# Optimization experiments

Measured on AMD Instinct MI355X. Metric: run time of the kernel, lower is better.

## Reference

```python
import jax, jax.numpy as jnp
import numpy as np

N, E, T, H, D_IN, D_OUT = 50000, 320000, 4, 4, 128, 128
NEG_SLOPE = 0.2
LN_EPS = 1e-5


def setup_inputs() -> dict:
    key = jax.random.key(0)
    ks = jax.random.split(key, 10)
    x = jax.random.normal(ks[0], (N, D_IN), jnp.float32)
    edge_index = jax.random.randint(ks[1], (2, E), 0, N, jnp.int32)
    edge_attr = jax.random.randint(ks[2], (E,), 0, T, jnp.int32)
    W_gat = jax.random.normal(ks[3], (T, D_IN, H * D_OUT), jnp.float32) / np.sqrt(D_IN)
    a_src = jax.random.normal(ks[4], (T, H, D_OUT), jnp.float32) / np.sqrt(D_OUT)
    a_dst = jax.random.normal(ks[5], (T, H, D_OUT), jnp.float32) / np.sqrt(D_OUT)
    b_gat = jnp.zeros((T, D_OUT), jnp.float32)
    edge_type_weights = jnp.ones((T,), jnp.float32) / T
    W_fuse = jax.random.normal(ks[6], (T * D_OUT, D_OUT), jnp.float32) / np.sqrt(T * D_OUT)
    b_fuse = jnp.zeros((D_OUT,), jnp.float32)
    ln_gamma = jnp.ones((D_OUT,), jnp.float32)
    ln_beta = jnp.zeros((D_OUT,), jnp.float32)
    return {"x": x, "edge_index": edge_index, "edge_attr": edge_attr,
            "W_gat": W_gat, "a_src": a_src, "a_dst": a_dst, "b_gat": b_gat,
            "edge_type_weights": edge_type_weights, "W_fuse": W_fuse,
            "b_fuse": b_fuse, "ln_gamma": ln_gamma, "ln_beta": ln_beta}


def _gat_one_type(x, src_all, dst_all, mask_all, W, a_s, a_d, b):
    # x: [N, D_in]; src_all/dst_all: [E+N] (type-mask + self-loops on all nodes)
    n = x.shape[0]
    h = (x @ W).reshape(n, H, D_OUT)                      # [N, H, D]
    alpha_s = jnp.sum(h * a_s, axis=-1)                   # [N, H]
    alpha_d = jnp.sum(h * a_d, axis=-1)                   # [N, H]
    logit = jax.nn.leaky_relu(alpha_s[src_all] + alpha_d[dst_all], NEG_SLOPE)  # [Ea, H]
    neg_inf = jnp.float32(-1e30)
    logit = jnp.where(mask_all[:, None], logit, neg_inf)
    m = jax.ops.segment_max(logit, dst_all, num_segments=n)   # [N, H] (self-loops ensure finite)
    ex = jnp.exp(logit - m[dst_all])
    ex = jnp.where(mask_all[:, None], ex, 0.0)
    denom = jax.ops.segment_sum(ex, dst_all, num_segments=n)  # [N, H]
    alpha = ex / denom[dst_all]                                # [Ea, H]
    msg = alpha[:, :, None] * h[src_all]                       # [Ea, H, D]
    out = jax.ops.segment_sum(msg, dst_all, num_segments=n)   # [N, H, D]
    return out.mean(axis=1) + b                                # concat=False -> head mean


def reference(x, edge_index, edge_attr, W_gat, a_src, a_dst, b_gat,
              edge_type_weights, W_fuse, b_fuse, ln_gamma, ln_beta):
    n = x.shape[0]
    self_idx = jnp.arange(n, dtype=edge_index.dtype)
    src_all = jnp.concatenate([edge_index[0], self_idx])
    dst_all = jnp.concatenate([edge_index[1], self_idx])
    outs = []
    for t in range(T):
        mask_all = jnp.concatenate([edge_attr == t, jnp.ones((n,), bool)])
        outs.append(_gat_one_type(x, src_all, dst_all, mask_all,
                                  W_gat[t], a_src[t], a_dst[t], b_gat[t]))
    w = jax.nn.softmax(edge_type_weights)
    x_cat = jnp.concatenate([outs[t] * w[t] for t in range(T)], axis=1)  # [N, T*D]
    y = x_cat @ W_fuse + b_fuse
    mu = jnp.mean(y, axis=-1, keepdims=True)
    var = jnp.var(y, axis=-1, keepdims=True)
    y = (y - mu) / jnp.sqrt(var + LN_EPS) * ln_gamma + ln_beta
    return jax.nn.relu(y)
```

## Files before the change

kernel.cpp:

```cpp
#include <hip/hip_runtime.h>
#include <hip/hip_bf16.h>

#define TT 4
#define HH 4
#define DD 128
#define KAGG 2048

typedef __attribute__((ext_vector_type(8))) short short8;
typedef __attribute__((ext_vector_type(4))) float f32x4;
typedef __attribute__((ext_vector_type(4))) unsigned int uint4v;

__device__ __forceinline__ float lrelu(float z) { return z > 0.f ? z : 0.2f * z; }
__device__ __forceinline__ float bf2f(unsigned short u) {
  union { unsigned int i; float f; } v; v.i = ((unsigned int)u) << 16; return v.f;
}
__device__ __forceinline__ unsigned short f2b(float f) {
  union { float f; unsigned int i; } u; u.f = f;
  unsigned int r = u.i + 0x7fff + ((u.i >> 16) & 1);
  return (unsigned short)(r >> 16);
}
__device__ __forceinline__ void unpack8v(uint4v u, float* hv) {
  hv[0] = bf2f((unsigned short)(u.x & 0xffff));
  hv[1] = bf2f((unsigned short)(u.x >> 16));
  hv[2] = bf2f((unsigned short)(u.y & 0xffff));
  hv[3] = bf2f((unsigned short)(u.y >> 16));
  hv[4] = bf2f((unsigned short)(u.z & 0xffff));
  hv[5] = bf2f((unsigned short)(u.z >> 16));
  hv[6] = bf2f((unsigned short)(u.w & 0xffff));
  hv[7] = bf2f((unsigned short)(u.w >> 16));
}

__global__ __launch_bounds__(256) void prologue_kernel(
    const float* __restrict__ x, unsigned short* __restrict__ xb, int total4,
    const float* __restrict__ Wg, const float* __restrict__ a_s,
    const float* __restrict__ a_d, const float* __restrict__ W_fuse,
    const float* __restrict__ b_gat, const float* __restrict__ etw,
    const float* __restrict__ b_fuse, unsigned short* __restrict__ Gfrag,
    unsigned short* __restrict__ Pall, float* __restrict__ cbias,
    const int* __restrict__ dst, const int* __restrict__ attr,
    int* __restrict__ deg, int E, int N) {
  int bid = blockIdx.x;
  const int nconv = (total4 + 255) >> 8;
  if (bid < nconv) {
    int i = bid * 256 + threadIdx.x;
    if (i < total4) {
      float4 v = ((const float4*)x)[i];
      ushort4 o;
      o.x = f2b(v.x); o.y = f2b(v.y); o.z = f2b(v.z); o.w = f2b(v.w);
      ((ushort4*)xb)[i] = o;
    }
    return;
  }
  bid -= nconv;
  if (bid < 1041) {
    float e0 = etw[0], e1 = etw[1], e2 = etw[2], e3 = etw[3];
    float mx = fmaxf(fmaxf(e0, e1), fmaxf(e2, e3));
    float w0 = __expf(e0 - mx), w1 = __expf(e1 - mx), w2 = __expf(e2 - mx),
          w3 = __expf(e3 - mx);
    float inv = 1.f / (w0 + w1 + w2 + w3);
    float wts[4] = {w0 * inv, w1 * inv, w2 * inv, w3 * inv};
    if (bid < 1024) {
      int idx = bid * 256 + threadIdx.x;
      int f = idx >> 9, l = (idx >> 3) & 63, j = idx & 7;
      int kt = f >> 5, kk = (f >> 3) & 3, n = f & 7;
      int K = kt * 128 + kk * 32 + (l >> 4) * 8 + j;
      int col = n * 16 + (l & 15);
      int t = K >> 9, head = (K >> 7) & 3, k = K & 127;
      const float* wr = Wg + (size_t)t * 65536 + k * 512 + head * 128;
      const float* wf = W_fuse + (size_t)t * 128 * 128 + col;
      float s = 0.f;
      for (int m = 0; m < 128; ++m) s += wr[m] * wf[(size_t)m * 128];
      Gfrag[idx] = f2b(0.25f * wts[t] * s);
    } else if (bid < 1040) {
      int idx = (bid - 1024) * 256 + threadIdx.x;
      int c = idx >> 7, k = idx & 127;
      int t = c >> 3, jj = c & 7, head = jj & 3;
      const float* av = ((jj < 4) ? a_s : a_d) + (t * 4 + head) * 128;
      const float* wr = Wg + (size_t)t * 65536 + k * 512 + head * 128;
      float s = 0.f;
      for (int m = 0; m < 128; ++m) s += wr[m] * av[m];
      Pall[c * 128 + k] = f2b(s);
    } else {
      int j = threadIdx.x;
      if (j < 128) {
        float s = b_fuse[j];
        for (int t = 0; t < 4; ++t) {
          float st = 0.f;
          for (int m = 0; m < 128; ++m)
            st += b_gat[t * 128 + m] * W_fuse[(size_t)(t * 128 + m) * 128 + j];
          s += wts[t] * st;
        }
        cbias[j] = s;
      }
    }
    return;
  }
  bid -= 1041;
  int e = bid * 256 + threadIdx.x;
  if (e < E) atomicAdd(&deg[attr[e] * N + dst[e]], 1);
}

__global__ __launch_bounds__(1024) void scanfused_kernel(
    const int* __restrict__ deg, int* __restrict__ rowptr,
    int* __restrict__ cursor, int* __restrict__ gcur, int M) {
  __shared__ int sh[1024];
  __shared__ int base;
  int i = blockIdx.x * 1024 + threadIdx.x;
  int v = (i < M) ? deg[i] : 0;
  sh[threadIdx.x] = v;
  __syncthreads();
  for (int off = 1; off < 1024; off <<= 1) {
    int xx = (threadIdx.x >= off) ? sh[threadIdx.x - off] : 0;
    __syncthreads();
    sh[threadIdx.x] += xx;
    __syncthreads();
  }
  if (threadIdx.x == 1023) base = atomicAdd(gcur, sh[1023]);
  __syncthreads();
  if (i < M) {
    int r = base + sh[threadIdx.x] - v;
    rowptr[i] = r;
    cursor[i] = r;
  }
}

__global__ __launch_bounds__(256) void scatter_alpha_kernel(
    const int* __restrict__ src, const int* __restrict__ dst,
    const int* __restrict__ attr, int* __restrict__ cursor,
    int* __restrict__ slist, const unsigned short* __restrict__ xb,
    const unsigned short* __restrict__ Pall, float* __restrict__ as_,
    float* __restrict__ ad_, int E, int N) {
  __shared__ uint4 ldsv[2048];
  int bid = blockIdx.x;
  const int nsc = (E + 255) >> 8;
  if (bid < nsc) {
    int e = bid * 256 + threadIdx.x;
    if (e < E) {
      int p = atomicAdd(&cursor[attr[e] * N + dst[e]], 1);
      slist[p] = src[e];
    }
    return;
  }
  bid -= nsc;
  unsigned char* lds = (unsigned char*)ldsv;
  const int n0 = bid * 128;
  const int tid = threadIdx.x, lane = tid & 63, wid = tid >> 6;
  const int lr = lane & 15, lg = lane >> 4;
#pragma unroll
  for (int i = 0; i < 8; ++i) {
    int chunk = tid + i * 256;
    int row = chunk >> 4, k16 = chunk & 15;
    int gr = n0 + row;
    uint4 v = make_uint4(0, 0, 0, 0);
    if (gr < N) v = *(const uint4*)(xb + (size_t)gr * DD + k16 * 8);
    *(uint4*)(lds + ((row * 256 + k16 * 16) ^ ((row & 7) << 4))) = v;
  }
  __syncthreads();
  f32x4 acc[2][2] = {};
#pragma unroll
  for (int kk = 0; kk < 4; ++kk) {
    short8 a[2], b[2];
#pragma unroll
    for (int m = 0; m < 2; ++m) {
      int row = wid * 32 + m * 16 + lr;
      a[m] = *(const short8*)(lds + ((row * 256 + kk * 64 + (lg << 4)) ^ ((row & 7) << 4)));
    }
#pragma unroll
    for (int n = 0; n < 2; ++n) {
      int c = n * 16 + lr;
      b[n] = *(const short8*)(Pall + c * DD + kk * 32 + lg * 8);
    }
#pragma unroll
    for (int m = 0; m < 2; ++m)
#pragma unroll
      for (int n = 0; n < 2; ++n)
        acc[m][n] = __builtin_amdgcn_mfma_f32_16x16x32_bf16(a[m], b[n], acc[m][n], 0, 0, 0);
  }
#pragma unroll
  for (int m = 0; m < 2; ++m)
#pragma unroll
    for (int n = 0; n < 2; ++n) {
      int c = n * 16 + lr;
      int t = c >> 3, jj = c & 7, head = jj & 3;
      float* dstp = (jj & 4) ? ad_ : as_;
#pragma unroll
      for (int r = 0; r < 4; ++r) {
        int gr = n0 + wid * 32 + m * 16 + lg * 4 + r;
        if (gr < N) dstp[((size_t)t * N + gr) * 4 + head] = acc[m][n][r];
      }
    }
}

__global__ __launch_bounds__(256) void gather_kernel(
    const int* __restrict__ slist, const int* __restrict__ rowptr,
    const int* __restrict__ deg, const float* __restrict__ as_,
    const float* __restrict__ ad_, const unsigned short* __restrict__ xb,
    unsigned short* __restrict__ AGG, int N) {
  int t = blockIdx.y;
  int lane = threadIdx.x & 63;
  int u = lane >> 4, c16 = lane & 15;
  int d = blockIdx.x * 16 + (threadIdx.x >> 6) * 4 + u;
  if (d >= N) return;
  size_t tn = (size_t)t * N;
  int dofs = c16 * 8;
  unsigned short* outp = AGG + (size_t)d * KAGG + t * 512 + dofs;

  int base = rowptr[tn + d], dg = deg[tn + d];
  uint4v uself = *(const uint4v*)(xb + (size_t)d * DD + dofs);
  if (dg == 0) {
#pragma unroll
    for (int h = 0; h < 4; ++h) *(uint4v*)(outp + h * DD) = uself;
    return;
  }

  float4 ad4 = *(const float4*)(ad_ + (tn + d) * 4);
  float4 av = *(const float4*)(as_ + (tn + d) * 4);
  float q[4], den[4], hv[8], acc[4][8];
  q[0] = __expf(lrelu(av.x + ad4.x));
  q[1] = __expf(lrelu(av.y + ad4.y));
  q[2] = __expf(lrelu(av.z + ad4.z));
  q[3] = __expf(lrelu(av.w + ad4.w));
  unpack8v(uself, hv);
#pragma unroll
  for (int h = 0; h < 4; ++h) {
    den[h] = q[h];
#pragma unroll
    for (int j = 0; j < 8; ++j) acc[h][j] = q[h] * hv[j];
  }

  int i = 0;
  for (; i + 1 < dg; i += 2) {
    int s0 = slist[base + i], s1 = slist[base + i + 1];
    float4 a0 = *(const float4*)(as_ + (tn + s0) * 4);
    float4 a1 = *(const float4*)(as_ + (tn + s1) * 4);
    uint4v u0 = *(const uint4v*)(xb + (size_t)s0 * DD + dofs);
    uint4v u1 = *(const uint4v*)(xb + (size_t)s1 * DD + dofs);
    float q0[4], q1[4];
    q0[0] = __expf(lrelu(a0.x + ad4.x));
    q0[1] = __expf(lrelu(a0.y + ad4.y));
    q0[2] = __expf(lrelu(a0.z + ad4.z));
    q0[3] = __expf(lrelu(a0.w + ad4.w));
    q1[0] = __expf(lrelu(a1.x + ad4.x));
    q1[1] = __expf(lrelu(a1.y + ad4.y));
    q1[2] = __expf(lrelu(a1.z + ad4.z));
    q1[3] = __expf(lrelu(a1.w + ad4.w));
#pragma unroll
    for (int h = 0; h < 4; ++h) den[h] += q0[h] + q1[h];
    unpack8v(u0, hv);
#pragma unroll
    for (int h = 0; h < 4; ++h)
#pragma unroll
      for (int j = 0; j < 8; ++j) acc[h][j] += q0[h] * hv[j];
    unpack8v(u1, hv);
#pragma unroll
    for (int h = 0; h < 4; ++h)
#pragma unroll
      for (int j = 0; j < 8; ++j) acc[h][j] += q1[h] * hv[j];
  }
  if (i < dg) {
    int s = slist[base + i];
    float4 a = *(const float4*)(as_ + (tn + s) * 4);
    uint4v ue = *(const uint4v*)(xb + (size_t)s * DD + dofs);
    float qe[4];
    qe[0] = __expf(lrelu(a.x + ad4.x));
    qe[1] = __expf(lrelu(a.y + ad4.y));
    qe[2] = __expf(lrelu(a.z + ad4.z));
    qe[3] = __expf(lrelu(a.w + ad4.w));
#pragma unroll
    for (int h = 0; h < 4; ++h) den[h] += qe[h];
    unpack8v(ue, hv);
#pragma unroll
    for (int h = 0; h < 4; ++h)
#pragma unroll
      for (int j = 0; j < 8; ++j) acc[h][j] += qe[h] * hv[j];
  }

#pragma unroll
  for (int h = 0; h < 4; ++h) {
    float r = 1.f / den[h];
    uint4v o;
    o.x = (unsigned)f2b(acc[h][0] * r) | ((unsigned)f2b(acc[h][1] * r) << 16);
    o.y = (unsigned)f2b(acc[h][2] * r) | ((unsigned)f2b(acc[h][3] * r) << 16);
    o.z = (unsigned)f2b(acc[h][4] * r) | ((unsigned)f2b(acc[h][5] * r) << 16);
    o.w = (unsigned)f2b(acc[h][6] * r) | ((unsigned)f2b(acc[h][7] * r) << 16);
    *(uint4v*)(outp + h * DD) = o;
  }
}

__global__ __launch_bounds__(256) void gemmln_kernel(
    const unsigned short* __restrict__ AGG, const unsigned short* __restrict__ Gfrag,
    const float* __restrict__ cbias, const float* __restrict__ gamma,
    const float* __restrict__ beta, float* __restrict__ out, int N) {
  __shared__ uint4 bbuf[2][2048];
  const int n0 = blockIdx.x * 128;
  const int tid = threadIdx.x, lane = tid & 63, wid = tid >> 6;
  const int lr = lane & 15, lg = lane >> 4;
  const int wrow = n0 + wid * 32;

  uint4 bn[8], an[8], ac[8];
#pragma unroll
  for (int i = 0; i < 8; ++i)
    bn[i] = *(const uint4*)(Gfrag + (size_t)(i * 256 + tid) * 8);
#pragma unroll
  for (int i = 0; i < 8; ++i) {
    int m = i >> 2, kk = i & 3;
    int gr = wrow + m * 16 + lr;
    an[i] = make_uint4(0, 0, 0, 0);
    if (gr < N) an[i] = *(const uint4*)(AGG + (size_t)gr * KAGG + kk * 32 + lg * 8);
  }
#pragma unroll
  for (int i = 0; i < 8; ++i) bbuf[0][i * 256 + tid] = bn[i];
  __syncthreads();
#pragma unroll
  for (int i = 0; i < 8; ++i) ac[i] = an[i];

  f32x4 acc[2][8] = {};
  int cur = 0;
  for (int kt = 0; kt < 16; ++kt) {
    if (kt < 15) {
#pragma unroll
      for (int i = 0; i < 8; ++i)
        bn[i] = *(const uint4*)(Gfrag + (size_t)(kt + 1) * 16384 + (size_t)(i * 256 + tid) * 8);
#pragma unroll
      for (int i = 0; i < 8; ++i) {
        int m = i >> 2, kk = i & 3;
        int gr = wrow + m * 16 + lr;
        an[i] = make_uint4(0, 0, 0, 0);
        if (gr < N)
          an[i] = *(const uint4*)(AGG + (size_t)gr * KAGG + (kt + 1) * 128 + kk * 32 + lg * 8);
      }
    }
    const unsigned char* lds = (const unsigned char*)bbuf[cur];
#pragma unroll
    for (int kk = 0; kk < 4; ++kk) {
      short8 a0 = *(const short8*)&ac[0 * 4 + kk];
      short8 a1 = *(const short8*)&ac[1 * 4 + kk];
#pragma unroll
      for (int n = 0; n < 8; ++n) {
        short8 b = *(const short8*)(lds + (kk * 8 + n) * 1024 + lane * 16);
        acc[0][n] = __builtin_amdgcn_mfma_f32_16x16x32_bf16(a0, b, acc[0][n], 0, 0, 0);
        acc[1][n] = __builtin_amdgcn_mfma_f32_16x16x32_bf16(a1, b, acc[1][n], 0, 0, 0);
      }
    }
    if (kt < 15) {
#pragma unroll
      for (int i = 0; i < 8; ++i) bbuf[cur ^ 1][i * 256 + tid] = bn[i];
      __syncthreads();
      cur ^= 1;
#pragma unroll
      for (int i = 0; i < 8; ++i) ac[i] = an[i];
    }
  }

  float cb[8], gm[8], bt[8];
#pragma unroll
  for (int n = 0; n < 8; ++n) {
    cb[n] = cbias[n * 16 + lr];
    gm[n] = gamma[n * 16 + lr];
    bt[n] = beta[n * 16 + lr];
  }
#pragma unroll
  for (int m = 0; m < 2; ++m)
#pragma unroll
    for (int rr = 0; rr < 4; ++rr) {
      float y[8];
      float s = 0.f, ss = 0.f;
#pragma unroll
      for (int n = 0; n < 8; ++n) {
        y[n] = acc[m][n][rr] + cb[n];
        s += y[n];
        ss += y[n] * y[n];
      }
#pragma unroll
      for (int mask = 1; mask <= 8; mask <<= 1) {
        s += __shfl_xor(s, mask);
        ss += __shfl_xor(ss, mask);
      }
      float mean = s * (1.f / 128.f);
      float var = ss * (1.f / 128.f) - mean * mean;
      float rstd = rsqrtf(var + 1e-5f);
      int gr = wrow + m * 16 + lg * 4 + rr;
      if (gr < N) {
#pragma unroll
        for (int n = 0; n < 8; ++n) {
          float v = (y[n] - mean) * rstd * gm[n] + bt[n];
          out[(size_t)gr * DD + n * 16 + lr] = fmaxf(0.f, v);
        }
      }
    }
}

extern "C" void kernel_launch(void* const* d_in, const int* in_sizes, int n_in,
                              void* d_out, int out_size, void* d_ws, size_t ws_size,
                              hipStream_t stream) {
  const float* x      = (const float*)d_in[0];
  const int*   ei     = (const int*)d_in[1];
  const int*   attr   = (const int*)d_in[2];
  const float* Wg     = (const float*)d_in[3];
  const float* a_src  = (const float*)d_in[4];
  const float* a_dst  = (const float*)d_in[5];
  const float* b_gat  = (const float*)d_in[6];
  const float* etw    = (const float*)d_in[7];
  const float* W_fuse = (const float*)d_in[8];
  const float* b_fuse = (const float*)d_in[9];
  const float* gamma  = (const float*)d_in[10];
  const float* beta   = (const float*)d_in[11];

  const int N = in_sizes[0] / DD;
  const int E = in_sizes[2];
  const int* src = ei;
  const int* dst = ei + E;
  const int M = TT * N;

  char* ws = (char*)d_ws;
  size_t off = 0;
  auto alloc = [&](size_t bytes) {
    void* p = ws + off;
    off += (bytes + 255) & ~(size_t)255;
    return p;
  };
  unsigned short* AGG   = (unsigned short*)alloc((size_t)N * KAGG * 2);
  unsigned short* xb    = (unsigned short*)alloc((size_t)N * DD * 2);
  unsigned short* Gfrag = (unsigned short*)alloc((size_t)512 * 512 * 2);
  unsigned short* Pall  = (unsigned short*)alloc((size_t)32 * DD * 2);
  float* cbias          = (float*)alloc(128 * sizeof(float));
  float* as_            = (float*)alloc((size_t)TT * N * 4 * sizeof(float));
  float* ad_            = (float*)alloc((size_t)TT * N * 4 * sizeof(float));
  int* deg              = (int*)alloc((size_t)(M + 1) * sizeof(int));
  int* rowptr           = (int*)alloc((size_t)M * sizeof(int));
  int* cursor           = (int*)alloc((size_t)M * sizeof(int));
  int* slist            = (int*)alloc((size_t)E * sizeof(int));

  hipMemsetAsync(deg, 0, (size_t)(M + 1) * sizeof(int), stream);

  int total4x = N * DD / 4;
  int nconv = (total4x + 255) / 256;
  int nhist = (E + 255) / 256;
  prologue_kernel<<<nconv + 1041 + nhist, 256, 0, stream>>>(
      x, xb, total4x, Wg, a_src, a_dst, W_fuse, b_gat, etw, b_fuse,
      Gfrag, Pall, cbias, dst, attr, deg, E, N);

  scanfused_kernel<<<(M + 1023) / 1024, 1024, 0, stream>>>(deg, rowptr, cursor,
                                                           deg + M, M);

  int nalpha = (N + 127) / 128;
  scatter_alpha_kernel<<<nhist + nalpha, 256, 0, stream>>>(
      src, dst, attr, cursor, slist, xb, Pall, as_, ad_, E, N);

  dim3 ggrid((N + 15) / 16, TT);
  gather_kernel<<<ggrid, 256, 0, stream>>>(slist, rowptr, deg, as_, ad_, xb, AGG, N);

  gemmln_kernel<<<(N + 127) / 128, 256, 0, stream>>>(AGG, Gfrag, cbias, gamma, beta,
                                                     (float*)d_out, N);
}
```

Measured before the change: 198.2 us.

## Split weight-fold into LDS-tiled kernel, unroll gather by four, single-buffer GEMM LDS

The folded W_gat·W_fuse product moves out of the prologue into a separate gprep kernel. That kernel stages each W_fuse slice in shared memory and computes 8 output rows per block with coalesced column access, replacing 262k threads that each did strided global reads. The gather loop is unrolled from 2 to 4 edges to issue more independent loads, with a scalar remainder loop. The GEMM+LayerNorm kernel drops its double-buffered LDS for a single buffer with two barriers per k-step. This halves LDS use, which may raise occupancy, but it serializes the LDS write against the MFMA reads.

New measurement: 275.0 us. +38.8%, slower.

```diff
diff --git a/kernel.cpp b/kernel.cpp
--- a/kernel.cpp
+++ b/kernel.cpp
@@ -35,10 +35,9 @@
     const float* __restrict__ Wg, const float* __restrict__ a_s,
     const float* __restrict__ a_d, const float* __restrict__ W_fuse,
     const float* __restrict__ b_gat, const float* __restrict__ etw,
-    const float* __restrict__ b_fuse, unsigned short* __restrict__ Gfrag,
-    unsigned short* __restrict__ Pall, float* __restrict__ cbias,
-    const int* __restrict__ dst, const int* __restrict__ attr,
-    int* __restrict__ deg, int E, int N) {
+    const float* __restrict__ b_fuse, unsigned short* __restrict__ Pall,
+    float* __restrict__ cbias, const int* __restrict__ dst,
+    const int* __restrict__ attr, int* __restrict__ deg, int E, int N) {
   int bid = blockIdx.x;
   const int nconv = (total4 + 255) >> 8;
   if (bid < nconv) {
@@ -52,27 +51,15 @@
     return;
   }
   bid -= nconv;
-  if (bid < 1041) {
+  if (bid < 17) {
     float e0 = etw[0], e1 = etw[1], e2 = etw[2], e3 = etw[3];
     float mx = fmaxf(fmaxf(e0, e1), fmaxf(e2, e3));
     float w0 = __expf(e0 - mx), w1 = __expf(e1 - mx), w2 = __expf(e2 - mx),
           w3 = __expf(e3 - mx);
     float inv = 1.f / (w0 + w1 + w2 + w3);
     float wts[4] = {w0 * inv, w1 * inv, w2 * inv, w3 * inv};
-    if (bid < 1024) {
+    if (bid < 16) {
       int idx = bid * 256 + threadIdx.x;
-      int f = idx >> 9, l = (idx >> 3) & 63, j = idx & 7;
-      int kt = f >> 5, kk = (f >> 3) & 3, n = f & 7;
-      int K = kt * 128 + kk * 32 + (l >> 4) * 8 + j;
-      int col = n * 16 + (l & 15);
-      int t = K >> 9, head = (K >> 7) & 3, k = K & 127;
-      const float* wr = Wg + (size_t)t * 65536 + k * 512 + head * 128;
-      const float* wf = W_fuse + (size_t)t * 128 * 128 + col;
-      float s = 0.f;
-      for (int m = 0; m < 128; ++m) s += wr[m] * wf[(size_t)m * 128];
-      Gfrag[idx] = f2b(0.25f * wts[t] * s);
-    } else if (bid < 1040) {
-      int idx = (bid - 1024) * 256 + threadIdx.x;
       int c = idx >> 7, k = idx & 127;
       int t = c >> 3, jj = c & 7, head = jj & 3;
       const float* av = ((jj < 4) ? a_s : a_d) + (t * 4 + head) * 128;
@@ -95,9 +82,46 @@
     }
     return;
   }
-  bid -= 1041;
+  bid -= 17;
   int e = bid * 256 + threadIdx.x;
   if (e < E) atomicAdd(&deg[attr[e] * N + dst[e]], 1);
+}
+
+__global__ __launch_bounds__(256) void gprep_kernel(
+    const float* __restrict__ Wg, const float* __restrict__ W_fuse,
+    const float* __restrict__ etw, unsigned short* __restrict__ Gfrag) {
+  __shared__ float Bs[128][128];
+  int t = blockIdx.x >> 6;
+  int kr0 = (blockIdx.x & 63) * 8;
+  const float* wf = W_fuse + (size_t)t * 16384;
+#pragma unroll
+  for (int i = 0; i < 64; ++i)
+    ((float*)Bs)[i * 256 + threadIdx.x] = wf[i * 256 + threadIdx.x];
+
+  float e0 = etw[0], e1 = etw[1], e2 = etw[2], e3 = etw[3];
+  float mx = fmaxf(fmaxf(e0, e1), fmaxf(e2, e3));
+  float w0 = __expf(e0 - mx), w1 = __expf(e1 - mx), w2 = __expf(e2 - mx),
+        w3 = __expf(e3 - mx);
+  float inv = 1.f / (w0 + w1 + w2 + w3);
+  float wt = ((t == 0) ? w0 : (t == 1) ? w1 : (t == 2) ? w2 : w3) * inv * 0.25f;
+  __syncthreads();
+
+  int rr = threadIdx.x >> 7;
+  int j  = threadIdx.x & 127;
+#pragma unroll
+  for (int r2 = 0; r2 < 4; ++r2) {
+    int kr = kr0 + r2 * 2 + rr;
+    int head = kr >> 7, k = kr & 127;
+    const float* wr = Wg + (size_t)t * 65536 + k * 512 + head * 128;
+    float s = 0.f;
+    for (int m = 0; m < 128; ++m) s += wr[m] * Bs[m][j];
+    s *= wt;
+    int K = t * 512 + kr;
+    int kt = K >> 7, kk = (K >> 5) & 3, n = j >> 4;
+    int f = (kt * 4 + kk) * 8 + n;
+    int lg = (K >> 3) & 3, lr = j & 15, j8 = K & 7;
+    Gfrag[(size_t)f * 512 + (lg * 16 + lr) * 8 + j8] = f2b(s);
+  }
 }
 
 __global__ __launch_bounds__(1024) void scanfused_kernel(
@@ -229,35 +253,59 @@
   }
 
   int i = 0;
-  for (; i + 1 < dg; i += 2) {
+  for (; i + 3 < dg; i += 4) {
     int s0 = slist[base + i], s1 = slist[base + i + 1];
+    int s2 = slist[base + i + 2], s3 = slist[base + i + 3];
     float4 a0 = *(const float4*)(as_ + (tn + s0) * 4);
     float4 a1 = *(const float4*)(as_ + (tn + s1) * 4);
+    float4 a2 = *(const float4*)(as_ + (tn + s2) * 4);
+    float4 a3 = *(const float4*)(as_ + (tn + s3) * 4);
     uint4v u0 = *(const uint4v*)(xb + (size_t)s0 * DD + dofs);
     uint4v u1 = *(const uint4v*)(xb + (size_t)s1 * DD + dofs);
-    float q0[4], q1[4];
-    q0[0] = __expf(lrelu(a0.x + ad4.x));
-    q0[1] = __expf(lrelu(a0.y + ad4.y));
-    q0[2] = __expf(lrelu(a0.z + ad4.z));
-    q0[3] = __expf(lrelu(a0.w + ad4.w));
-    q1[0] = __expf(lrelu(a1.x + ad4.x));
-    q1[1] = __expf(lrelu(a1.y + ad4.y));
-    q1[2] = __expf(lrelu(a1.z + ad4.z));
-    q1[3] = __expf(lrelu(a1.w + ad4.w));
-#pragma unroll
-    for (int h = 0; h < 4; ++h) den[h] += q0[h] + q1[h];
+    uint4v u2 = *(const uint4v*)(xb + (size_t)s2 * DD + dofs);
+    uint4v u3 = *(const uint4v*)(xb + (size_t)s3 * DD + dofs);
+    float qq[4][4];
+    qq[0][0] = __expf(lrelu(a0.x + ad4.x));
+    qq[0][1] = __expf(lrelu(a0.y + ad4.y));
+    qq[0][2] = __expf(lrelu(a0.z + ad4.z));
+    qq[0][3] = __expf(lrelu(a0.w + ad4.w));
+    qq[1][0] = __expf(lrelu(a1.x + ad4.x));
+    qq[1][1] = __expf(lrelu(a1.y + ad4.y));
+    qq[1][2] = __expf(lrelu(a1.z + ad4.z));
+    qq[1][3] = __expf(lrelu(a1.w + ad4.w));
+    qq[2][0] = __expf(lrelu(a2.x + ad4.x));
+    qq[2][1] = __expf(lrelu(a2.y + ad4.y));
+    qq[2][2] = __expf(lrelu(a2.z + ad4.z));
+    qq[2][3] = __expf(lrelu(a2.w + ad4.w));
+    qq[3][0] = __expf(lrelu(a3.x + ad4.x));
+    qq[3][1] = __expf(lrelu(a3.y + ad4.y));
+    qq[3][2] = __expf(lrelu(a3.z + ad4.z));
+    qq[3][3] = __expf(lrelu(a3.w + ad4.w));
+#pragma unroll
+    for (int h = 0; h < 4; ++h)
+      den[h] += qq[0][h] + qq[1][h] + qq[2][h] + qq[3][h];
     unpack8v(u0, hv);
 #pragma unroll
     for (int h = 0; h < 4; ++h)
 #pragma unroll
-      for (int j = 0; j < 8; ++j) acc[h][j] += q0[h] * hv[j];
+      for (int j = 0; j < 8; ++j) acc[h][j] += qq[0][h] * hv[j];
     unpack8v(u1, hv);
 #pragma unroll
     for (int h = 0; h < 4; ++h)
 #pragma unroll
-      for (int j = 0; j < 8; ++j) acc[h][j] += q1[h] * hv[j];
-  }
-  if (i < dg) {
+      for (int j = 0; j < 8; ++j) acc[h][j] += qq[1][h] * hv[j];
+    unpack8v(u2, hv);
+#pragma unroll
+    for (int h = 0; h < 4; ++h)
+#pragma unroll
+      for (int j = 0; j < 8; ++j) acc[h][j] += qq[2][h] * hv[j];
+    unpack8v(u3, hv);
+#pragma unroll
+    for (int h = 0; h < 4; ++h)
+#pragma unroll
+      for (int j = 0; j < 8; ++j) acc[h][j] += qq[3][h] * hv[j];
+  }
+  for (; i < dg; ++i) {
     int s = slist[base + i];
     float4 a = *(const float4*)(as_ + (tn + s) * 4);
     uint4v ue = *(const uint4v*)(xb + (size_t)s * DD + dofs);
@@ -291,7 +339,7 @@
     const unsigned short* __restrict__ AGG, const unsigned short* __restrict__ Gfrag,
     const float* __restrict__ cbias, const float* __restrict__ gamma,
     const float* __restrict__ beta, float* __restrict__ out, int N) {
-  __shared__ uint4 bbuf[2][2048];
+  __shared__ uint4 bbuf[2048];
   const int n0 = blockIdx.x * 128;
   const int tid = threadIdx.x, lane = tid & 63, wid = tid >> 6;
   const int lr = lane & 15, lg = lane >> 4;
@@ -309,13 +357,12 @@
     if (gr < N) an[i] = *(const uint4*)(AGG + (size_t)gr * KAGG + kk * 32 + lg * 8);
   }
 #pragma unroll
-  for (int i = 0; i < 8; ++i) bbuf[0][i * 256 + tid] = bn[i];
+  for (int i = 0; i < 8; ++i) bbuf[i * 256 + tid] = bn[i];
+#pragma unroll
+  for (int i = 0; i < 8; ++i) ac[i] = an[i];
   __syncthreads();
-#pragma unroll
-  for (int i = 0; i < 8; ++i) ac[i] = an[i];
 
   f32x4 acc[2][8] = {};
-  int cur = 0;
   for (int kt = 0; kt < 16; ++kt) {
     if (kt < 15) {
 #pragma unroll
@@ -330,7 +377,7 @@
           an[i] = *(const uint4*)(AGG + (size_t)gr * KAGG + (kt + 1) * 128 + kk * 32 + lg * 8);
       }
     }
-    const unsigned char* lds = (const unsigned char*)bbuf[cur];
+    const unsigned char* lds = (const unsigned char*)bbuf;
 #pragma unroll
     for (int kk = 0; kk < 4; ++kk) {
       short8 a0 = *(const short8*)&ac[0 * 4 + kk];
@@ -343,12 +390,12 @@
       }
     }
     if (kt < 15) {
-#pragma unroll
-      for (int i = 0; i < 8; ++i) bbuf[cur ^ 1][i * 256 + tid] = bn[i];
       __syncthreads();
-      cur ^= 1;
+#pragma unroll
+      for (int i = 0; i < 8; ++i) bbuf[i * 256 + tid] = bn[i];
 #pragma unroll
       for (int i = 0; i < 8; ++i) ac[i] = an[i];
+      __syncthreads();
     }
   }
 
@@ -436,9 +483,11 @@
   int total4x = N * DD / 4;
   int nconv = (total4x + 255) / 256;
   int nhist = (E + 255) / 256;
-  prologue_kernel<<<nconv + 1041 + nhist, 256, 0, stream>>>(
+  prologue_kernel<<<nconv + 17 + nhist, 256, 0, stream>>>(
       x, xb, total4x, Wg, a_src, a_dst, W_fuse, b_gat, etw, b_fuse,
-      Gfrag, Pall, cbias, dst, attr, deg, E, N);
+      Pall, cbias, dst, attr, deg, E, N);
+
+  gprep_kernel<<<256, 256, 0, stream>>>(Wg, W_fuse, etw, Gfrag);
 
   scanfused_kernel<<<(M + 1023) / 1024, 1024, 0, stream>>>(deg, rowptr, cursor,
                                                            deg + M, M);
```
